# Performance work log

Measured on AMD Instinct MI355X. Metric: run time of the kernel, lower is better.

Reference implementation:

```python
import jax, jax.numpy as jnp
import numpy as np

B, C, H, W = 8, 256, 64, 64
GROUPS = 32
EPS = 1e-5


def setup_inputs() -> dict:
    key = jax.random.key(0)
    ks = jax.random.split(key, 6)
    s = 1.0 / np.sqrt(C)
    return {
        "x": jax.random.normal(ks[0], (B, C, H, W), dtype=jnp.float32),
        "gn_w": jnp.ones((C,), jnp.float32),
        "gn_b": jnp.zeros((C,), jnp.float32),
        "wq": jax.random.normal(ks[1], (C, C), jnp.float32) * s,
        "bq": jnp.zeros((C,), jnp.float32),
        "wk": jax.random.normal(ks[2], (C, C), jnp.float32) * s,
        "bk": jnp.zeros((C,), jnp.float32),
        "wv": jax.random.normal(ks[3], (C, C), jnp.float32) * s,
        "bv": jnp.zeros((C,), jnp.float32),
        "wo": jax.random.normal(ks[4], (C, C), jnp.float32) * s,
        "bo": jnp.zeros((C,), jnp.float32),
    }


def group_norm(x, w, b):
    # x: [B, C, H, W]; normalize over (C//GROUPS, H, W) per group
    Bn, Cn, Hn, Wn = x.shape
    xg = x.reshape(Bn, GROUPS, Cn // GROUPS, Hn, Wn)
    mu = jnp.mean(xg, axis=(2, 3, 4), keepdims=True)
    var = jnp.var(xg, axis=(2, 3, 4), keepdims=True)
    xn = (xg - mu) * jax.lax.rsqrt(var + EPS)
    xn = xn.reshape(Bn, Cn, Hn, Wn)
    return xn * w[None, :, None, None] + b[None, :, None, None]


def reference(x, gn_w, gn_b, wq, bq, wk, bk, wv, bv, wo, bo):
    Bn, Cn, Hn, Wn = x.shape
    h = group_norm(x, gn_w, gn_b)
    hf = h.reshape(Bn, Cn, Hn * Wn)  # [B, C, N]
    # 1x1 conv == channel matmul; produce tokens-major [B, N, C]
    q = jnp.einsum('bcn,oc->bno', hf, wq) + bq  # [B, N, C]
    k = jnp.einsum('bcn,oc->bon', hf, wk) + bk[None, :, None]  # [B, C, N]
    v = jnp.einsum('bcn,oc->bno', hf, wv) + bv  # [B, N, C]
    alpha = jnp.einsum('bnc,bcm->bnm', q, k) / jnp.sqrt(jnp.float32(Cn))
    alpha = jax.nn.softmax(alpha, axis=-1)  # [B, N, N]
    out = jnp.einsum('bnm,bmc->bnc', alpha, v)  # [B, N, C]
    out = jnp.einsum('bnc,oc->bon', out, wo) + bo[None, :, None]  # [B, C, N]
    return out.reshape(Bn, Cn, Hn, Wn) + x
```

## Files before the change

### kernel.cpp

```cpp
#include <hip/hip_runtime.h>
#include <hip/hip_bf16.h>
#include <cstdint>


typedef short short8 __attribute__((ext_vector_type(8)));
typedef float f32x16 __attribute__((ext_vector_type(16)));

__device__ __forceinline__ unsigned short f2bf(float f){
  uint32_t u = __builtin_bit_cast(uint32_t, f);
  u += 0x7FFFu + ((u >> 16) & 1u);
  return (unsigned short)(u >> 16);
}
__device__ __forceinline__ uint32_t pk2(float a, float b){
  return (uint32_t)f2bf(a) | ((uint32_t)f2bf(b) << 16);
}
__device__ __forceinline__ void gload16(const void* g, void* l){
  auto gp = reinterpret_cast<uint32_t __attribute__((address_space(1)))*>(
      reinterpret_cast<uintptr_t>(g));
  auto lp = reinterpret_cast<uint32_t __attribute__((address_space(3)))*>(
      reinterpret_cast<uintptr_t>(l));
  __builtin_amdgcn_global_load_lds(gp, lp, 16, 0, 0);
}

__global__ void cvt_w_kernel(const float* wq, const float* wk, const float* wv, const float* wo,
                             ushort* wqb, ushort* wkb, ushort* wvb, ushort* wob){
  int i = blockIdx.x*256 + threadIdx.x;
  wqb[i]=f2bf(wq[i]); wkb[i]=f2bf(wk[i]); wvb[i]=f2bf(wv[i]); wob[i]=f2bf(wo[i]);
}

__global__ void gn_stats_kernel(const float* __restrict__ x, float* __restrict__ gst){
  int bg = blockIdx.x;
  const float* p = x + (size_t)bg*32768;
  float s=0.f, sq=0.f;
  for(int i=threadIdx.x;i<32768;i+=256){ float v=p[i]; s+=v; sq+=v*v; }
  #pragma unroll
  for(int o=32;o>0;o>>=1){ s+=__shfl_down(s,o); sq+=__shfl_down(sq,o); }
  __shared__ float ls[4], lq[4];
  if((threadIdx.x&63)==0){ ls[threadIdx.x>>6]=s; lq[threadIdx.x>>6]=sq; }
  __syncthreads();
  if(threadIdx.x==0){
    s=ls[0]+ls[1]+ls[2]+ls[3]; sq=lq[0]+lq[1]+lq[2]+lq[3];
    float mu=s*(1.f/32768.f);
    float var=sq*(1.f/32768.f)-mu*mu;
    gst[bg*2]=mu; gst[bg*2+1]=rsqrtf(var+1e-5f);
  }
}

__global__ void gn_apply_kernel(const float* __restrict__ x, const float* __restrict__ gw,
                                const float* __restrict__ gb, const float* __restrict__ gst,
                                ushort* __restrict__ ht){
  int nt=blockIdx.x, ct=blockIdx.y, b=blockIdx.z;
  int n0=nt*64, c0=ct*32;
  __shared__ float tile[32][65];
  __shared__ float smu[4], srs[4], sw[32], sb[32];
  int tid=threadIdx.x;
  if(tid<4){ int g=(c0>>3)+tid; smu[tid]=gst[(b*32+g)*2]; srs[tid]=gst[(b*32+g)*2+1]; }
  if(tid<32){ sw[tid]=gw[c0+tid]; sb[tid]=gb[c0+tid]; }
  __syncthreads();
  int ci=tid>>3, j0=(tid&7)*8;
  const float* xp = x + ((size_t)(b*256)+c0+ci)*4096 + n0 + j0;
  float mu=smu[ci>>3], rs=srs[ci>>3], w=sw[ci], bb=sb[ci];
  #pragma unroll
  for(int j=0;j<8;j++){ tile[ci][j0+j]=(xp[j]-mu)*rs*w+bb; }
  __syncthreads();
  int nl=tid>>2, oct=tid&3;
  union{ ushort u[8]; uint4 v; } o;
  #pragma unroll
  for(int j=0;j<8;j++) o.u[j]=f2bf(tile[oct*8+j][nl]);
  *reinterpret_cast<uint4*>(ht + ((size_t)(b*4096)+n0+nl)*256 + c0 + oct*8) = o.v;
}

template<int BIAS_ROW>
__global__ __launch_bounds__(256,2) void gemm_km(const ushort* __restrict__ A, const ushort* __restrict__ Bm,
         ushort* __restrict__ D, const float* __restrict__ bias, float scale, int ldd){
  __shared__ ushort Al[128*64];
  __shared__ ushort Bl[128*64];
  int m0=blockIdx.x*128, n0=blockIdx.y*128;
  int tid=threadIdx.x, w=tid>>6, lane=tid&63, ln=lane&31, hi=lane>>5;
  f32x16 acc[2][2];
  #pragma unroll
  for(int a=0;a<2;a++)
    #pragma unroll
    for(int c=0;c<2;c++)
      #pragma unroll
      for(int r=0;r<16;r++) acc[a][c][r]=0.f;
  for(int kt=0;kt<4;kt++){
    __syncthreads();
    #pragma unroll
    for(int i=0;i<4;i++){
      int idx=i*256+tid; int row=idx>>3; int chs=(idx^row)&7;
      gload16(A + (size_t)(m0+row)*256 + kt*64 + chs*8, (char*)Al + (i*256+w*64)*16);
    }
    #pragma unroll
    for(int i=0;i<4;i++){
      int idx=i*256+tid; int row=idx>>3; int chs=(idx^row)&7;
      gload16(Bm + (size_t)(n0+row)*256 + kt*64 + chs*8, (char*)Bl + (i*256+w*64)*16);
    }
    __syncthreads();
    #pragma unroll
    for(int kk=0;kk<4;kk++){
      short8 af[2], bfr[2];
      #pragma unroll
      for(int t=0;t<2;t++){
        int ra=(w>>1)*64+t*32+ln; int ca=((kk*2+hi)^ra)&7;
        af[t]=*reinterpret_cast<const short8*>(Al + ra*64 + ca*8);
        int rb=(w&1)*64+t*32+ln; int cb=((kk*2+hi)^rb)&7;
        bfr[t]=*reinterpret_cast<const short8*>(Bl + rb*64 + cb*8);
      }
      #pragma unroll
      for(int ti=0;ti<2;ti++)
        #pragma unroll
        for(int tj=0;tj<2;tj++)
          acc[ti][tj]=__builtin_amdgcn_mfma_f32_32x32x16_bf16(af[ti],bfr[tj],acc[ti][tj],0,0,0);
    }
  }
  #pragma unroll
  for(int ti=0;ti<2;ti++){
    #pragma unroll
    for(int tj=0;tj<2;tj++){
      int col=n0+(w&1)*64+tj*32+ln;
      float bc = BIAS_ROW? 0.f : bias[col];
      #pragma unroll
      for(int r=0;r<16;r++){
        int row=m0+(w>>1)*64+ti*32+(r&3)+8*(r>>2)+4*hi;
        float v=acc[ti][tj][r] + (BIAS_ROW? bias[row]: bc);
        D[(size_t)row*ldd+col]=f2bf(v*scale);
      }
    }
  }
}

__global__ __launch_bounds__(512,2) void attn_kernel(
    const ushort* __restrict__ qb, const ushort* __restrict__ kb,
    const ushort* __restrict__ vtb, const ushort* __restrict__ wob,
    const float* __restrict__ bo, const float* __restrict__ x,
    float* __restrict__ out){
  __shared__ ushort Kl[64*256];
  __shared__ ushort Vl[256*64];
  __shared__ float exch[8][64*32];
  __shared__ float ml[8][2][32];
  int tid=threadIdx.x, w=tid>>6, lane=tid&63, ln=lane&31, hi=lane>>5;
  int qg=w&3, h=w>>2;
  int b=blockIdx.y, n0=blockIdx.x*128+qg*32;
  int n=n0+ln;
  short8 qf[16];
  {
    const ushort* qrow = qb + ((size_t)(b*4096)+n)*256 + hi*8;
    #pragma unroll
    for(int kc=0;kc<16;kc++) qf[kc]=*reinterpret_cast<const short8*>(qrow+kc*16);
  }
  f32x16 oacc[8];
  #pragma unroll
  for(int i=0;i<8;i++)
    #pragma unroll
    for(int r=0;r<16;r++) oacc[i][r]=0.f;
  float M=-3.0e38f, L=0.f;
  const ushort* kbp = kb + (size_t)b*4096*256;
  const ushort* vbp = vtb + (size_t)b*4096;

  for(int t=0;t<64;t++){
    __syncthreads();
    #pragma unroll
    for(int i=0;i<4;i++){
      int idx=i*512+tid; int row=idx>>5, ch=idx&31;
      int chs=(ch&24)|((ch^row)&7);
      gload16(kbp + (size_t)(t*64+row)*256 + chs*8, (char*)Kl + (i*512+w*64)*16);
    }
    #pragma unroll
    for(int i=0;i<4;i++){
      int idx=i*512+tid; int row=idx>>3; int chs=(idx^row)&7;
      gload16(vbp + (size_t)row*32768 + t*64 + chs*8, (char*)Vl + (i*512+w*64)*16);
    }
    __syncthreads();
    f32x16 s;
    #pragma unroll
    for(int r=0;r<16;r++) s[r]=0.f;
    int kr=h*32+ln;
    const ushort* klr = Kl + kr*256;
    #pragma unroll
    for(int kc=0;kc<16;kc++){
      int cw=kc*2+hi; int chs=(cw&24)|((cw^kr)&7);
      short8 a=*reinterpret_cast<const short8*>(klr+chs*8);
      s=__builtin_amdgcn_mfma_f32_32x32x16_bf16(a,qf[kc],s,0,0,0);
    }
    float tmax=s[0];
    #pragma unroll
    for(int r=1;r<16;r++) tmax=fmaxf(tmax,s[r]);
    tmax=fmaxf(tmax,__shfl_xor(tmax,32));
    float Mn=fmaxf(M,tmax);
    float sc=__expf(M-Mn);
    float p[16]; float ts=0.f;
    #pragma unroll
    for(int r=0;r<16;r++){ p[r]=__expf(s[r]-Mn); ts+=p[r]; }
    ts+=__shfl_xor(ts,32);
    L=L*sc+ts; M=Mn;
    #pragma unroll
    for(int i=0;i<8;i++)
      #pragma unroll
      for(int r=0;r<16;r++) oacc[i][r]*=sc;
    short8 pa[2];
    #pragma unroll
    for(int ks=0;ks<2;ks++){
      uint32_t c01=pk2(p[ks*8+0],p[ks*8+1]);
      uint32_t c23=pk2(p[ks*8+2],p[ks*8+3]);
      uint32_t c45=pk2(p[ks*8+4],p[ks*8+5]);
      uint32_t c67=pk2(p[ks*8+6],p[ks*8+7]);
      uint32_t x01=(uint32_t)__shfl_xor((int)c01,32), x23=(uint32_t)__shfl_xor((int)c23,32);
      uint32_t x45=(uint32_t)__shfl_xor((int)c45,32), x67=(uint32_t)__shfl_xor((int)c67,32);
      union{ uint32_t u[4]; short8 v; } r_;
      r_.u[0]= hi? x45:c01;
      r_.u[1]= hi? x67:c23;
      r_.u[2]= hi? c45:x01;
      r_.u[3]= hi? c67:x23;
      pa[ks]=r_.v;
    }
    #pragma unroll
    for(int ct=0;ct<8;ct++){
      int c=ct*32+ln;
      const ushort* vlr = Vl + c*64;
      #pragma unroll
      for(int ks=0;ks<2;ks++){
        int cw=h*4+ks*2+hi; int chs=cw^(c&7);
        short8 a=*reinterpret_cast<const short8*>(vlr+chs*8);
        oacc[ct]=__builtin_amdgcn_mfma_f32_32x32x16_bf16(a,pa[ks],oacc[ct],0,0,0);
      }
    }
  }
  __syncthreads();
  if(hi==0){ ml[w][0][ln]=M; ml[w][1][ln]=L; }
  __syncthreads();
  float Mp=ml[w^4][0][ln], Lp=ml[w^4][1][ln];
  float Mt=fmaxf(M,Mp);
  float fo=__expf(M-Mt), fpp=__expf(Mp-Mt);
  float g=fo/(fo*L+fpp*Lp);
  #pragma unroll
  for(int i=0;i<8;i++)
    #pragma unroll
    for(int r=0;r<16;r++) oacc[i][r]*=g;
  short8 obf[16];
  #pragma unroll
  for(int cb=0;cb<4;cb++){
    __syncthreads();
    float* ex=&exch[w][0];
    #pragma unroll
    for(int u=0;u<2;u++){
      int ct=cb*2+u;
      #pragma unroll
      for(int r=0;r<16;r++){
        int cl=u*32+(r&3)+8*(r>>2)+4*hi;
        ex[cl*32+ln]=oacc[ct][r];
      }
    }
    __syncthreads();
    const float* exq=&exch[w^4][0];
    #pragma unroll
    for(int u=0;u<2;u++){
      int ct=cb*2+u;
      #pragma unroll
      for(int r=0;r<16;r++){
        int cl=u*32+(r&3)+8*(r>>2)+4*hi;
        oacc[ct][r]+=exq[cl*32+ln];
      }
    }
    #pragma unroll
    for(int kq=0;kq<4;kq++){
      int ct=cb*2+(kq>>1); int rb=(kq&1)*8;
      uint32_t c01=pk2(oacc[ct][rb+0],oacc[ct][rb+1]);
      uint32_t c23=pk2(oacc[ct][rb+2],oacc[ct][rb+3]);
      uint32_t c45=pk2(oacc[ct][rb+4],oacc[ct][rb+5]);
      uint32_t c67=pk2(oacc[ct][rb+6],oacc[ct][rb+7]);
      uint32_t x01=(uint32_t)__shfl_xor((int)c01,32), x23=(uint32_t)__shfl_xor((int)c23,32);
      uint32_t x45=(uint32_t)__shfl_xor((int)c45,32), x67=(uint32_t)__shfl_xor((int)c67,32);
      union{ uint32_t u[4]; short8 v; } r_;
      r_.u[0]= hi? x45:c01;
      r_.u[1]= hi? x67:c23;
      r_.u[2]= hi? c45:x01;
      r_.u[3]= hi? c67:x23;
      obf[cb*4+kq]=r_.v;
    }
  }
  #pragma unroll
  for(int cot=0;cot<4;cot++){
    f32x16 d;
    #pragma unroll
    for(int r=0;r<16;r++) d[r]=0.f;
    int coa=h*128+cot*32+ln;
    const ushort* wr=wob+(size_t)coa*256+hi*8;
    #pragma unroll
    for(int kbv=0;kbv<16;kbv++){
      short8 a=*reinterpret_cast<const short8*>(wr+kbv*16);
      d=__builtin_amdgcn_mfma_f32_32x32x16_bf16(a,obf[kbv],d,0,0,0);
    }
    #pragma unroll
    for(int r=0;r<16;r++){
      int co=h*128+cot*32+(r&3)+8*(r>>2)+4*hi;
      size_t oi=((size_t)(b*256)+co)*4096 + n0+ln;
      out[oi]=d[r]+bo[co]+x[oi];
    }
  }
}

extern "C" void kernel_launch(void* const* d_in, const int* in_sizes, int n_in,
                              void* d_out, int out_size, void* d_ws, size_t ws_size,
                              hipStream_t stream){
  const float* x   =(const float*)d_in[0];
  const float* gw  =(const float*)d_in[1];
  const float* gb  =(const float*)d_in[2];
  const float* wq  =(const float*)d_in[3];
  const float* bq  =(const float*)d_in[4];
  const float* wk  =(const float*)d_in[5];
  const float* bk  =(const float*)d_in[6];
  const float* wv  =(const float*)d_in[7];
  const float* bv  =(const float*)d_in[8];
  const float* wo  =(const float*)d_in[9];
  const float* bo  =(const float*)d_in[10];
  float* out=(float*)d_out;
  char* ws=(char*)d_ws;
  const size_t SZ = (size_t)32768*256*2;
  ushort* ht =(ushort*)(ws);
  ushort* qb =(ushort*)(ws+SZ);
  ushort* kb2=(ushort*)(ws+2*SZ);
  ushort* vtb=(ushort*)(ws+3*SZ);
  ushort* wqb=(ushort*)(ws+4*SZ);
  ushort* wkb=(ushort*)(ws+4*SZ+131072);
  ushort* wvb=(ushort*)(ws+4*SZ+262144);
  ushort* wob=(ushort*)(ws+4*SZ+393216);
  float*  gst=(float*) (ws+4*SZ+524288);

  cvt_w_kernel<<<256,256,0,stream>>>(wq,wk,wv,wo,wqb,wkb,wvb,wob);
  gn_stats_kernel<<<256,256,0,stream>>>(x,gst);
  gn_apply_kernel<<<dim3(64,8,8),256,0,stream>>>(x,gw,gb,gst,ht);
  gemm_km<0><<<dim3(256,2),256,0,stream>>>(ht,wqb,qb,bq,0.0625f,256);
  gemm_km<0><<<dim3(256,2),256,0,stream>>>(ht,wkb,kb2,bk,1.0f,256);
  gemm_km<1><<<dim3(2,256),256,0,stream>>>(wvb,ht,vtb,bv,1.0f,32768);
  attn_kernel<<<dim3(32,8),512,0,stream>>>(qb,kb2,vtb,wob,bo,x,out);
}
```

Before: 392.0 us.

## Double-buffer attention K/V loads, add lazy softmax rescale, fuse Q/K projections

The attention loop now double-buffers K/V tiles in shared memory, prefetching the next tile while the current one is computed, and synchronises with explicit vmcnt waits and barriers. The online softmax works in base 2, with log2(e) folded into the Q scale, and only rescales the accumulators when the running max grows by more than a threshold. Probability and output packing to bf16 now truncates instead of rounding. Q and K projections share a single GEMM kernel that loads A once. Truncation and lazy rescaling add a small precision risk, and the fused GEMM uses more shared memory per block.

```diff
diff --git a/kernel.cpp b/kernel.cpp
--- a/kernel.cpp
+++ b/kernel.cpp
@@ -11,8 +11,8 @@
   u += 0x7FFFu + ((u >> 16) & 1u);
   return (unsigned short)(u >> 16);
 }
-__device__ __forceinline__ uint32_t pk2(float a, float b){
-  return (uint32_t)f2bf(a) | ((uint32_t)f2bf(b) << 16);
+__device__ __forceinline__ uint32_t pk2t(float a, float b){
+  return (__builtin_bit_cast(uint32_t,a)>>16) | (__builtin_bit_cast(uint32_t,b)&0xFFFF0000u);
 }
 __device__ __forceinline__ void gload16(const void* g, void* l){
   auto gp = reinterpret_cast<uint32_t __attribute__((address_space(1)))*>(
@@ -70,9 +70,78 @@
   *reinterpret_cast<uint4*>(ht + ((size_t)(b*4096)+n0+nl)*256 + c0 + oct*8) = o.v;
 }
 
-template<int BIAS_ROW>
-__global__ __launch_bounds__(256,2) void gemm_km(const ushort* __restrict__ A, const ushort* __restrict__ Bm,
-         ushort* __restrict__ D, const float* __restrict__ bias, float scale, int ldd){
+__global__ __launch_bounds__(256,2) void gemm_qk(const ushort* __restrict__ A,
+         const ushort* __restrict__ Bq, const ushort* __restrict__ Bk,
+         ushort* __restrict__ Dq, ushort* __restrict__ Dk,
+         const float* __restrict__ bq, const float* __restrict__ bk, float qscale){
+  __shared__ ushort Al[128*64];
+  __shared__ ushort Bql[128*64];
+  __shared__ ushort Bkl[128*64];
+  int m0=blockIdx.x*128, n0=blockIdx.y*128;
+  int tid=threadIdx.x, w=tid>>6, lane=tid&63, ln=lane&31, hi=lane>>5;
+  f32x16 aq[2][2], ak[2][2];
+  #pragma unroll
+  for(int a=0;a<2;a++)
+    #pragma unroll
+    for(int c=0;c<2;c++)
+      #pragma unroll
+      for(int r=0;r<16;r++){ aq[a][c][r]=0.f; ak[a][c][r]=0.f; }
+  for(int kt=0;kt<4;kt++){
+    __syncthreads();
+    #pragma unroll
+    for(int i=0;i<4;i++){
+      int idx=i*256+tid; int row=idx>>3; int chs=(idx^row)&7;
+      gload16(A  + (size_t)(m0+row)*256 + kt*64 + chs*8, (char*)Al  + (i*256+w*64)*16);
+    }
+    #pragma unroll
+    for(int i=0;i<4;i++){
+      int idx=i*256+tid; int row=idx>>3; int chs=(idx^row)&7;
+      gload16(Bq + (size_t)(n0+row)*256 + kt*64 + chs*8, (char*)Bql + (i*256+w*64)*16);
+    }
+    #pragma unroll
+    for(int i=0;i<4;i++){
+      int idx=i*256+tid; int row=idx>>3; int chs=(idx^row)&7;
+      gload16(Bk + (size_t)(n0+row)*256 + kt*64 + chs*8, (char*)Bkl + (i*256+w*64)*16);
+    }
+    __syncthreads();
+    #pragma unroll
+    for(int kk=0;kk<4;kk++){
+      short8 af[2], bqf[2], bkf[2];
+      #pragma unroll
+      for(int t=0;t<2;t++){
+        int ra=(w>>1)*64+t*32+ln; int ca=((kk*2+hi)^ra)&7;
+        af[t]=*reinterpret_cast<const short8*>(Al + ra*64 + ca*8);
+        int rb=(w&1)*64+t*32+ln; int cb=((kk*2+hi)^rb)&7;
+        bqf[t]=*reinterpret_cast<const short8*>(Bql + rb*64 + cb*8);
+        bkf[t]=*reinterpret_cast<const short8*>(Bkl + rb*64 + cb*8);
+      }
+      #pragma unroll
+      for(int ti=0;ti<2;ti++)
+        #pragma unroll
+        for(int tj=0;tj<2;tj++){
+          aq[ti][tj]=__builtin_amdgcn_mfma_f32_32x32x16_bf16(af[ti],bqf[tj],aq[ti][tj],0,0,0);
+          ak[ti][tj]=__builtin_amdgcn_mfma_f32_32x32x16_bf16(af[ti],bkf[tj],ak[ti][tj],0,0,0);
+        }
+    }
+  }
+  #pragma unroll
+  for(int ti=0;ti<2;ti++){
+    #pragma unroll
+    for(int tj=0;tj<2;tj++){
+      int col=n0+(w&1)*64+tj*32+ln;
+      float bqc=bq[col], bkc=bk[col];
+      #pragma unroll
+      for(int r=0;r<16;r++){
+        int row=m0+(w>>1)*64+ti*32+(r&3)+8*(r>>2)+4*hi;
+        Dq[(size_t)row*256+col]=f2bf((aq[ti][tj][r]+bqc)*qscale);
+        Dk[(size_t)row*256+col]=f2bf(ak[ti][tj][r]+bkc);
+      }
+    }
+  }
+}
+
+__global__ __launch_bounds__(256,2) void gemm_vt(const ushort* __restrict__ A, const ushort* __restrict__ Bm,
+         ushort* __restrict__ D, const float* __restrict__ bias){
   __shared__ ushort Al[128*64];
   __shared__ ushort Bl[128*64];
   int m0=blockIdx.x*128, n0=blockIdx.y*128;
@@ -119,12 +188,10 @@
     #pragma unroll
     for(int tj=0;tj<2;tj++){
       int col=n0+(w&1)*64+tj*32+ln;
-      float bc = BIAS_ROW? 0.f : bias[col];
       #pragma unroll
       for(int r=0;r<16;r++){
         int row=m0+(w>>1)*64+ti*32+(r&3)+8*(r>>2)+4*hi;
-        float v=acc[ti][tj][r] + (BIAS_ROW? bias[row]: bc);
-        D[(size_t)row*ldd+col]=f2bf(v*scale);
+        D[(size_t)row*32768+col]=f2bf(acc[ti][tj][r]+bias[row]);
       }
     }
   }
@@ -135,10 +202,9 @@
     const ushort* __restrict__ vtb, const ushort* __restrict__ wob,
     const float* __restrict__ bo, const float* __restrict__ x,
     float* __restrict__ out){
-  __shared__ ushort Kl[64*256];
-  __shared__ ushort Vl[256*64];
-  __shared__ float exch[8][64*32];
+  __shared__ ushort smem[2][32768];
   __shared__ float ml[8][2][32];
+  float* exch = reinterpret_cast<float*>(&smem[0][0]);
   int tid=threadIdx.x, w=tid>>6, lane=tid&63, ln=lane&31, hi=lane>>5;
   int qg=w&3, h=w>>2;
   int b=blockIdx.y, n0=blockIdx.x*128+qg*32;
@@ -158,53 +224,74 @@
   const ushort* kbp = kb + (size_t)b*4096*256;
   const ushort* vbp = vtb + (size_t)b*4096;
 
-  for(int t=0;t<64;t++){
-    __syncthreads();
+  auto stage=[&](int t1, int bufi){
+    char* Kd=(char*)&smem[bufi][0];
+    char* Vd=(char*)&smem[bufi][16384];
     #pragma unroll
     for(int i=0;i<4;i++){
       int idx=i*512+tid; int row=idx>>5, ch=idx&31;
       int chs=(ch&24)|((ch^row)&7);
-      gload16(kbp + (size_t)(t*64+row)*256 + chs*8, (char*)Kl + (i*512+w*64)*16);
+      gload16(kbp + (size_t)(t1*64+row)*256 + chs*8, Kd + (i*512+w*64)*16);
     }
     #pragma unroll
     for(int i=0;i<4;i++){
       int idx=i*512+tid; int row=idx>>3; int chs=(idx^row)&7;
-      gload16(vbp + (size_t)row*32768 + t*64 + chs*8, (char*)Vl + (i*512+w*64)*16);
-    }
-    __syncthreads();
+      gload16(vbp + (size_t)row*32768 + t1*64 + chs*8, Vd + (i*512+w*64)*16);
+    }
+  };
+
+  stage(0, 0);
+
+  for(int t=0;t<64;t++){
+    int cur=t&1;
+    if(t<63){
+      stage(t+1, cur^1);
+      asm volatile("s_waitcnt vmcnt(8)" ::: "memory");
+    } else {
+      asm volatile("s_waitcnt vmcnt(0)" ::: "memory");
+    }
+    asm volatile("s_barrier" ::: "memory");
+    const ushort* kBase=&smem[cur][0];
+    const ushort* vBase=&smem[cur][16384];
     f32x16 s;
     #pragma unroll
     for(int r=0;r<16;r++) s[r]=0.f;
     int kr=h*32+ln;
-    const ushort* klr = Kl + kr*256;
+    const ushort* klr = kBase + kr*256;
     #pragma unroll
     for(int kc=0;kc<16;kc++){
       int cw=kc*2+hi; int chs=(cw&24)|((cw^kr)&7);
       short8 a=*reinterpret_cast<const short8*>(klr+chs*8);
       s=__builtin_amdgcn_mfma_f32_32x32x16_bf16(a,qf[kc],s,0,0,0);
     }
-    float tmax=s[0];
-    #pragma unroll
-    for(int r=1;r<16;r++) tmax=fmaxf(tmax,s[r]);
+    float tmax=fmaxf(fmaxf(fmaxf(s[0],s[1]),fmaxf(s[2],s[3])),
+                     fmaxf(fmaxf(s[4],s[5]),fmaxf(s[6],s[7])));
+    float tmax2=fmaxf(fmaxf(fmaxf(s[8],s[9]),fmaxf(s[10],s[11])),
+                      fmaxf(fmaxf(s[12],s[13]),fmaxf(s[14],s[15])));
+    tmax=fmaxf(tmax,tmax2);
     tmax=fmaxf(tmax,__shfl_xor(tmax,32));
-    float Mn=fmaxf(M,tmax);
-    float sc=__expf(M-Mn);
+    if(__any(tmax > M + 8.f)){
+      float Mn=fmaxf(M,tmax);
+      float sc=exp2f(M-Mn);
+      L*=sc;
+      #pragma unroll
+      for(int i=0;i<8;i++)
+        #pragma unroll
+        for(int r=0;r<16;r++) oacc[i][r]*=sc;
+      M=Mn;
+    }
     float p[16]; float ts=0.f;
     #pragma unroll
-    for(int r=0;r<16;r++){ p[r]=__expf(s[r]-Mn); ts+=p[r]; }
+    for(int r=0;r<16;r++){ p[r]=exp2f(s[r]-M); ts+=p[r]; }
     ts+=__shfl_xor(ts,32);
-    L=L*sc+ts; M=Mn;
-    #pragma unroll
-    for(int i=0;i<8;i++)
-      #pragma unroll
-      for(int r=0;r<16;r++) oacc[i][r]*=sc;
+    L+=ts;
     short8 pa[2];
     #pragma unroll
     for(int ks=0;ks<2;ks++){
-      uint32_t c01=pk2(p[ks*8+0],p[ks*8+1]);
-      uint32_t c23=pk2(p[ks*8+2],p[ks*8+3]);
-      uint32_t c45=pk2(p[ks*8+4],p[ks*8+5]);
-      uint32_t c67=pk2(p[ks*8+6],p[ks*8+7]);
+      uint32_t c01=pk2t(p[ks*8+0],p[ks*8+1]);
+      uint32_t c23=pk2t(p[ks*8+2],p[ks*8+3]);
+      uint32_t c45=pk2t(p[ks*8+4],p[ks*8+5]);
+      uint32_t c67=pk2t(p[ks*8+6],p[ks*8+7]);
       uint32_t x01=(uint32_t)__shfl_xor((int)c01,32), x23=(uint32_t)__shfl_xor((int)c23,32);
       uint32_t x45=(uint32_t)__shfl_xor((int)c45,32), x67=(uint32_t)__shfl_xor((int)c67,32);
       union{ uint32_t u[4]; short8 v; } r_;
@@ -217,7 +304,7 @@
     #pragma unroll
     for(int ct=0;ct<8;ct++){
       int c=ct*32+ln;
-      const ushort* vlr = Vl + c*64;
+      const ushort* vlr = vBase + c*64;
       #pragma unroll
       for(int ks=0;ks<2;ks++){
         int cw=h*4+ks*2+hi; int chs=cw^(c&7);
@@ -225,13 +312,14 @@
         oacc[ct]=__builtin_amdgcn_mfma_f32_32x32x16_bf16(a,pa[ks],oacc[ct],0,0,0);
       }
     }
+    asm volatile("s_barrier" ::: "memory");
   }
   __syncthreads();
   if(hi==0){ ml[w][0][ln]=M; ml[w][1][ln]=L; }
   __syncthreads();
   float Mp=ml[w^4][0][ln], Lp=ml[w^4][1][ln];
   float Mt=fmaxf(M,Mp);
-  float fo=__expf(M-Mt), fpp=__expf(Mp-Mt);
+  float fo=exp2f(M-Mt), fpp=exp2f(Mp-Mt);
   float g=fo/(fo*L+fpp*Lp);
   #pragma unroll
   for(int i=0;i<8;i++)
@@ -241,7 +329,7 @@
   #pragma unroll
   for(int cb=0;cb<4;cb++){
     __syncthreads();
-    float* ex=&exch[w][0];
+    float* ex=exch + w*2048;
     #pragma unroll
     for(int u=0;u<2;u++){
       int ct=cb*2+u;
@@ -252,7 +340,7 @@
       }
     }
     __syncthreads();
-    const float* exq=&exch[w^4][0];
+    const float* exq=exch + (w^4)*2048;
     #pragma unroll
     for(int u=0;u<2;u++){
       int ct=cb*2+u;
@@ -265,10 +353,10 @@
     #pragma unroll
     for(int kq=0;kq<4;kq++){
       int ct=cb*2+(kq>>1); int rb=(kq&1)*8;
-      uint32_t c01=pk2(oacc[ct][rb+0],oacc[ct][rb+1]);
-      uint32_t c23=pk2(oacc[ct][rb+2],oacc[ct][rb+3]);
-      uint32_t c45=pk2(oacc[ct][rb+4],oacc[ct][rb+5]);
-      uint32_t c67=pk2(oacc[ct][rb+6],oacc[ct][rb+7]);
+      uint32_t c01=pk2t(oacc[ct][rb+0],oacc[ct][rb+1]);
+      uint32_t c23=pk2t(oacc[ct][rb+2],oacc[ct][rb+3]);
+      uint32_t c45=pk2t(oacc[ct][rb+4],oacc[ct][rb+5]);
+      uint32_t c67=pk2t(oacc[ct][rb+6],oacc[ct][rb+7]);
       uint32_t x01=(uint32_t)__shfl_xor((int)c01,32), x23=(uint32_t)__shfl_xor((int)c23,32);
       uint32_t x45=(uint32_t)__shfl_xor((int)c45,32), x67=(uint32_t)__shfl_xor((int)c67,32);
       union{ uint32_t u[4]; short8 v; } r_;
@@ -330,8 +418,7 @@
   cvt_w_kernel<<<256,256,0,stream>>>(wq,wk,wv,wo,wqb,wkb,wvb,wob);
   gn_stats_kernel<<<256,256,0,stream>>>(x,gst);
   gn_apply_kernel<<<dim3(64,8,8),256,0,stream>>>(x,gw,gb,gst,ht);
-  gemm_km<0><<<dim3(256,2),256,0,stream>>>(ht,wqb,qb,bq,0.0625f,256);
-  gemm_km<0><<<dim3(256,2),256,0,stream>>>(ht,wkb,kb2,bk,1.0f,256);
-  gemm_km<1><<<dim3(2,256),256,0,stream>>>(wvb,ht,vtb,bv,1.0f,32768);
+  gemm_qk<<<dim3(256,2),256,0,stream>>>(ht,wqb,wkb,qb,kb2,bq,bk,0.090168439f);
+  gemm_vt<<<dim3(2,256),256,0,stream>>>(wvb,ht,vtb,bv);
   attn_kernel<<<dim3(32,8),512,0,stream>>>(qb,kb2,vtb,wob,bo,x,out);
 }
```

Result: faster. 362.5 us (-7.5%).
